# Kernel tuning notes

Hardware: AMD Instinct MI355X
Metric: run time of the kernel (lower is better)

The kernel has to match this reference:

```python
import jax, jax.numpy as jnp
import numpy as np
import math

DIM = 512
HEADS = 8          # dim // num_head_channels = 512 // 64
HEAD_CH = 64
GROUPS = 32        # guided-diffusion normalization() = GroupNorm(32, dim)
EPS = 1e-5
CROSS_DIM = 768


def setup_inputs() -> dict:
    key = jax.random.key(0)
    ks = jax.random.split(key, 8)
    B, C, Hs, Ws, L = 16, DIM, 32, 32, 77
    x = jax.random.normal(ks[0], (B, C, Hs, Ws), dtype=jnp.float32)
    c = jax.random.normal(ks[1], (B, CROSS_DIM, L), dtype=jnp.float32)
    # GroupNorm affine params
    gamma = jnp.ones((C,), jnp.float32)
    beta = jnp.zeros((C,), jnp.float32)
    # 1x1 conv weights stored as [out, in]
    w_qkv = jax.random.normal(ks[2], (3 * C, C), jnp.float32) / math.sqrt(C)
    b_qkv = jnp.zeros((3 * C,), jnp.float32)
    w_c = jax.random.normal(ks[3], (2 * C, CROSS_DIM), jnp.float32) / math.sqrt(CROSS_DIM)
    b_c = jnp.zeros((2 * C,), jnp.float32)
    # NOTE: original proj_out is zero-initialized (zero_module); we use small
    # random weights so the reference exercises non-trivial math end-to-end.
    w_p = jax.random.normal(ks[4], (C, C), jnp.float32) / math.sqrt(C)
    b_p = jnp.zeros((C,), jnp.float32)
    return {"x": x, "c": c, "gamma": gamma, "beta": beta,
            "w_qkv": w_qkv, "b_qkv": b_qkv, "w_c": w_c, "b_c": b_c,
            "w_p": w_p, "b_p": b_p}


def reference(x, c, gamma, beta, w_qkv, b_qkv, w_c, b_c, w_p, b_p):
    B, C, Hs, Ws = x.shape
    T = Hs * Ws
    xf = x.reshape(B, C, T)

    # GroupNorm(32) over (channels_per_group, spatial)
    xg = xf.reshape(B, GROUPS, C // GROUPS, T)
    mean = xg.mean(axis=(2, 3), keepdims=True)
    var = xg.var(axis=(2, 3), keepdims=True)
    xn = ((xg - mean) * jax.lax.rsqrt(var + EPS)).reshape(B, C, T)
    xn = xn * gamma[None, :, None] + beta[None, :, None]

    # qkv 1x1 conv: [B, 3C, T]
    qkv = jnp.einsum('oc,bct->bot', w_qkv, xn) + b_qkv[None, :, None]
    q, k, v = jnp.split(qkv, 3, axis=1)
    q = q.reshape(B, HEADS, HEAD_CH, T)
    k = k.reshape(B, HEADS, HEAD_CH, T)
    v = v.reshape(B, HEADS, HEAD_CH, T)

    # cross-attn cond kv: [B, 2C, L] -> concat on sequence axis
    ckv = jnp.einsum('oc,bcl->bol', w_c, c) + b_c[None, :, None]
    kc, vc = jnp.split(ckv, 2, axis=1)
    L = c.shape[-1]
    k = jnp.concatenate([k, kc.reshape(B, HEADS, HEAD_CH, L)], axis=-1)
    v = jnp.concatenate([v, vc.reshape(B, HEADS, HEAD_CH, L)], axis=-1)

    scale = 1.0 / math.sqrt(HEAD_CH)
    # scores [B, H, T, T+L]; scale applied inside softmax as in FusedSoftmaxMaybeApex
    logits = jnp.einsum('bhct,bhcs->bhts', q, k) * scale
    w = jax.nn.softmax(logits, axis=-1)
    a = jnp.einsum('bhts,bhcs->bhct', w, v).reshape(B, C, T)

    h = jnp.einsum('oc,bct->bot', w_p, a) + b_p[None, :, None]
    return (xf + h).reshape(B, C, Hs, Ws)
```

## Files before the change

kernel.cpp:

```cpp
#include <hip/hip_runtime.h>

#define B_   16
#define C_   512
#define T_   1024
#define H_   8
#define D_   64
#define G_   32
#define L_   77
#define S_   1101
#define SPAD 1152
#define NPAD 51
#define CD_  768
#define BT_  (B_*T_)
#define SROW 72
#define QSC  0.18033688011112042f

typedef __bf16 bf16x8 __attribute__((ext_vector_type(8)));
typedef float  f32x4  __attribute__((ext_vector_type(4)));

static __device__ __forceinline__ unsigned short f2bf(float f) {
    unsigned int u = __float_as_uint(f);
    u = (u + 0x7fffu + ((u >> 16) & 1u)) >> 16;
    return (unsigned short)u;
}

static __device__ __forceinline__ unsigned int pk_bf16(float a, float b) {
    unsigned int d;
    asm("v_cvt_pk_bf16_f32 %0, %1, %2" : "=v"(d) : "v"(a), "v"(b));
    return d;
}

static __device__ __forceinline__ void gload_lds16(const unsigned short* g,
                                                   unsigned short* l) {
    __builtin_amdgcn_global_load_lds(
        (const __attribute__((address_space(1))) unsigned int*)g,
        (__attribute__((address_space(3))) unsigned int*)l, 16, 0, 0);
}

__global__ __launch_bounds__(256) void prep_k(const float* __restrict__ x,
                                              float* __restrict__ stats,
                                              const float* __restrict__ w_qkv,
                                              const float* __restrict__ w_p,
                                              const float* __restrict__ w_c,
                                              const float* __restrict__ cin,
                                              unsigned short* __restrict__ wqkv_pk,
                                              unsigned short* __restrict__ wp_pk,
                                              unsigned short* __restrict__ wc_pk,
                                              unsigned short* __restrict__ cpk) {
    const int tid = threadIdx.x;
    if (blockIdx.x < 512) {
        const int bg = blockIdx.x;
        const float* p = x + (size_t)bg * 16384;
        float s = 0.f, s2 = 0.f;
        for (int i = tid; i < 16384; i += 256) {
            float v = p[i];
            s += v; s2 += v * v;
        }
        __shared__ float rs[256], rs2[256];
        rs[tid] = s; rs2[tid] = s2;
        __syncthreads();
        for (int off = 128; off > 0; off >>= 1) {
            if (tid < off) { rs[tid] += rs[tid + off]; rs2[tid] += rs2[tid + off]; }
            __syncthreads();
        }
        if (tid == 0) {
            float mean = rs[0] * (1.0f / 16384.0f);
            float var  = rs2[0] * (1.0f / 16384.0f) - mean * mean;
            stats[2 * bg]     = mean;
            stats[2 * bg + 1] = rsqrtf(var + 1e-5f);
        }
        return;
    }
    if (blockIdx.x < 1408) {
        const int cid = (blockIdx.x - 512) * 256 + tid;
        const float* src;
        unsigned short* dst;
        if (cid < 98304) {
            const int ml = cid & 127, k8 = (cid >> 7) & 7, kt = (cid >> 10) & 7, mt = cid >> 13;
            src = w_qkv + (size_t)(mt * 128 + ml) * 512 + kt * 64 + k8 * 8;
            dst = wqkv_pk + (size_t)cid * 8;
        } else if (cid < 131072) {
            const int c2 = cid - 98304;
            const int ml = c2 & 127, k8 = (c2 >> 7) & 7, kt = (c2 >> 10) & 7, mt = c2 >> 13;
            src = w_p + (size_t)(mt * 128 + ml) * 512 + kt * 64 + k8 * 8;
            dst = wp_pk + (size_t)c2 * 8;
        } else {
            const int c3 = cid - 131072;
            const int ml = c3 & 127, k8 = (c3 >> 7) & 7;
            const int ktmt = c3 >> 10;
            const int kt = ktmt % 12, mt = ktmt / 12;
            src = w_c + (size_t)(mt * 128 + ml) * 768 + kt * 64 + k8 * 8;
            dst = wc_pk + (size_t)c3 * 8;
        }
        const float4 v0 = *(const float4*)src, v1 = *(const float4*)(src + 4);
        unsigned short tmp[8];
        tmp[0] = f2bf(v0.x); tmp[1] = f2bf(v0.y); tmp[2] = f2bf(v0.z); tmp[3] = f2bf(v0.w);
        tmp[4] = f2bf(v1.x); tmp[5] = f2bf(v1.y); tmp[6] = f2bf(v1.z); tmp[7] = f2bf(v1.w);
        *(uint4*)dst = *(uint4*)tmp;
        return;
    }
    const int idx2 = blockIdx.x - 1408;
    const int kt = idx2 % 12, b = idx2 / 12;
#pragma unroll
    for (int it = 0; it < 4; it++) {
        const int idx = it * 256 + tid;
        const int k8 = idx >> 7, l = idx & 127;
        unsigned short tmp[8];
        const float* src = cin + ((size_t)b * CD_ + kt * 64 + k8 * 8) * L_ + l;
#pragma unroll
        for (int q = 0; q < 8; q++)
            tmp[q] = (l < L_) ? f2bf(src[(size_t)q * L_]) : (unsigned short)0;
        *(uint4*)&cpk[(size_t)b * 98304 + ((size_t)(kt * 8 + k8)) * 1024 + (size_t)l * 8] =
            *(uint4*)tmp;
    }
}

__global__ __launch_bounds__(256) void gn_apply_t(const float* __restrict__ x,
                                                  const float* __restrict__ stats,
                                                  const float* __restrict__ gamma,
                                                  const float* __restrict__ beta,
                                                  unsigned short* __restrict__ xnT) {
    const int t0 = blockIdx.x * 64, kt = blockIdx.y, b = blockIdx.z;
    const int c0 = kt * 64;
    const int tid = threadIdx.x;
    __shared__ float st[64][66];
#pragma unroll
    for (int it = 0; it < 4; it++) {
        const int fid = it * 256 + tid;
        const int ci = fid >> 4, t4 = (fid & 15) * 4;
        const int c = c0 + ci;
        const float4 xv = *(const float4*)&x[((size_t)(b * C_ + c) << 10) + t0 + t4];
        const int bg = b * G_ + (c >> 4);
        const float mean = stats[2 * bg], istd = stats[2 * bg + 1];
        const float gs = gamma[c] * istd, gb = beta[c] - mean * gs;
        st[t4 + 0][ci] = xv.x * gs + gb;
        st[t4 + 1][ci] = xv.y * gs + gb;
        st[t4 + 2][ci] = xv.z * gs + gb;
        st[t4 + 3][ci] = xv.w * gs + gb;
    }
    __syncthreads();
#pragma unroll
    for (int it = 0; it < 2; it++) {
        const int cid = it * 256 + tid;
        const int k8 = cid >> 6, tl = cid & 63;
        const int n = (b << 10) + t0 + tl;
        const int nt = n >> 7, nm = n & 127;
        unsigned short tmp[8];
        const float* src = &st[tl][k8 * 8];
#pragma unroll
        for (int q = 0; q < 8; q++) tmp[q] = f2bf(src[q]);
        *(uint4*)&xnT[(((size_t)nt * 8 + kt) * 8 + k8) * 1024 + (size_t)nm * 8] = *(uint4*)tmp;
    }
}

template<int MODE, int KT>
__global__ __launch_bounds__(256) void mgemm_k(const unsigned short* __restrict__ Apk,
                                               const unsigned short* __restrict__ Bpk,
                                               const float* __restrict__ bias,
                                               const float* __restrict__ resid,
                                               unsigned short* __restrict__ qpk,
                                               unsigned short* __restrict__ kpk,
                                               unsigned short* __restrict__ vpk,
                                               float* __restrict__ outp) {
    __shared__ unsigned short lds[18432];
    const int tid = threadIdx.x, wave = tid >> 6, lane = tid & 63;
    const int quad = lane >> 4, l16 = lane & 15;
    const int nt = blockIdx.x, mt = blockIdx.y;
    const int mw = (wave & 1) * 64, nw = (wave >> 1) * 64;

    f32x4 acc[4][4];
#pragma unroll
    for (int i = 0; i < 4; i++)
#pragma unroll
        for (int j = 0; j < 4; j++) acc[i][j] = (f32x4){0.f, 0.f, 0.f, 0.f};

    const unsigned short* Ab = Apk + (size_t)mt * KT * 8192;
    const unsigned short* Bb = Bpk + ((MODE == 2) ? (size_t)blockIdx.z * KT * 8192 : 0)
                                   + (size_t)nt * KT * 8192;

    for (int kt = 0; kt < KT; kt++) {
        const unsigned short* as = Ab + kt * 8192 + wave * 2048 + lane * 8;
        const unsigned short* bs = Bb + kt * 8192 + wave * 2048 + lane * 8;
        unsigned short* la = lds + wave * 2048;
        unsigned short* lb = lds + 8192 + wave * 2048;
#pragma unroll
        for (int j = 0; j < 4; j++) {
            gload_lds16(as + j * 512, la + j * 512);
            gload_lds16(bs + j * 512, lb + j * 512);
        }
        __syncthreads();
#pragma unroll
        for (int kh = 0; kh < 2; kh++) {
            const int k8 = kh * 4 + quad;
            bf16x8 af[4], bfr[4];
#pragma unroll
            for (int i = 0; i < 4; i++) {
                af[i]  = *(const bf16x8*)&lds[(size_t)(k8 * 128 + mw + i * 16 + l16) * 8];
                bfr[i] = *(const bf16x8*)&lds[8192 + (size_t)(k8 * 128 + nw + i * 16 + l16) * 8];
            }
#pragma unroll
            for (int mi = 0; mi < 4; mi++)
#pragma unroll
                for (int ni = 0; ni < 4; ni++)
                    acc[mi][ni] = __builtin_amdgcn_mfma_f32_16x16x32_bf16(
                        af[mi], bfr[ni], acc[mi][ni], 0, 0, 0);
        }
        __syncthreads();
    }

    const int gm0 = mt * 128 + mw;
    const int gn0 = nt * 128 + nw;

    if (MODE == 1) {
        const int b = gn0 >> 10, t0 = gn0 & 1023;
#pragma unroll
        for (int mi = 0; mi < 4; mi++) {
#pragma unroll
            for (int r = 0; r < 4; r++) {
                const int m = gm0 + mi * 16 + quad * 4 + r;
                const float bv = bias[m];
                const size_t rowb = ((size_t)(b * C_ + m) << 10) + t0;
#pragma unroll
                for (int ni = 0; ni < 4; ni++) {
                    const size_t a = rowb + ni * 16 + l16;
                    outp[a] = acc[mi][ni][r] + bv + resid[a];
                }
            }
        }
        return;
    }

    const int region = gm0 >> 9;
    const int h = (gm0 & 511) >> 6;
    const int b = (MODE == 2) ? blockIdx.z : (gn0 >> 10);
    const int bh = b * 8 + h;
    const bool vregion = (MODE == 0) ? (region == 2) : (region == 1);

    if (!vregion) {
        const float sc = (MODE == 0 && region == 0) ? QSC : 1.0f;
        unsigned short* base;
        int trow0;
        size_t tilestride;
        if (MODE == 0) {
            base = (region == 0) ? qpk + (size_t)bh * 16 * 4096
                                 : kpk + (size_t)bh * 18 * 4096;
            trow0 = gn0 & 1023;
        } else {
            base = kpk + (size_t)(bh * 18 + 16 + (gn0 >> 6)) * 4096;
            trow0 = -1;
        }
        (void)tilestride;
#pragma unroll
        for (int mi = 0; mi < 4; mi++) {
            const int k8 = mi * 2 + (quad >> 1);
            const int sub = (quad & 1) * 4;
#pragma unroll
            for (int ni = 0; ni < 4; ni++) {
                float vv[4];
                bool valid = true;
                if (MODE == 2) valid = (gn0 + ni * 16 + l16) < L_;
#pragma unroll
                for (int r = 0; r < 4; r++)
                    vv[r] = valid ? (acc[mi][ni][r] + bias[gm0 + mi * 16 + quad * 4 + r]) * sc
                                  : 0.f;
                uint2 d;
                d.x = pk_bf16(vv[0], vv[1]);
                d.y = pk_bf16(vv[2], vv[3]);
                unsigned short* dst;
                if (MODE == 0) {
                    const int t = trow0 + ni * 16 + l16;
                    dst = base + (size_t)(t >> 6) * 4096 + ((size_t)k8 * 64 + (t & 63)) * 8 + sub;
                } else {
                    const int row = ni * 16 + l16;
                    dst = base + ((size_t)k8 * 64 + row) * 8 + sub;
                }
                *(uint2*)dst = d;
            }
        }
    } else {
        unsigned short* wlds = lds + wave * 4608;
#pragma unroll
        for (int mi = 0; mi < 4; mi++)
#pragma unroll
            for (int ni = 0; ni < 4; ni++) {
                bool valid = true;
                if (MODE == 2) valid = (gn0 + ni * 16 + l16) < L_;
#pragma unroll
                for (int r = 0; r < 4; r++) {
                    const float v = valid ? acc[mi][ni][r] + bias[gm0 + mi * 16 + quad * 4 + r]
                                          : 0.f;
                    wlds[(mi * 16 + quad * 4 + r) * SROW + ni * 16 + l16] = f2bf(v);
                }
            }
        __syncthreads();
        const int stile = (MODE == 0) ? ((gn0 & 1023) >> 6) : (16 + (gn0 >> 6));
        unsigned short* dst = vpk + (size_t)(bh * 18 + stile) * 4096;
        const int sk8 = lane & 7, cb = lane >> 3;
#pragma unroll
        for (int it = 0; it < 8; it++) {
            const int ch = it * 8 + cb;
            *(uint4*)&dst[((size_t)sk8 * 64 + ch) * 8] =
                *(const uint4*)&wlds[ch * SROW + sk8 * 8];
        }
    }
}

__global__ __launch_bounds__(256, 4) void flash_k(const unsigned short* __restrict__ qpk,
                                                  const unsigned short* __restrict__ kpk,
                                                  const unsigned short* __restrict__ vpk,
                                                  unsigned short* __restrict__ aT) {
    __shared__ __align__(16) unsigned short ks[4096];
    __shared__ __align__(16) unsigned short vs[4096];
    __shared__ __align__(16) unsigned short psA[4 * 32 * SROW];

    const int tid  = threadIdx.x;
    const int wave = tid >> 6, lane = tid & 63;
    const int quad = lane >> 4, l16 = lane & 15;
    const int bh  = blockIdx.x;
    const int b = bh >> 3, h = bh & 7;
    const int qt0 = blockIdx.y * 128;

    const unsigned short* qtb = qpk + ((size_t)bh * 16 + blockIdx.y * 2 + (wave >> 1)) * 4096;
    const int qr0 = (wave & 1) * 32 + l16;
    bf16x8 bq0[2], bq1[2];
#pragma unroll
    for (int s = 0; s < 2; s++) {
        bq0[s] = *(const bf16x8*)&qtb[((size_t)quad * 64 + qr0 + s * 16) * 8];
        bq1[s] = *(const bf16x8*)&qtb[((size_t)(quad + 4) * 64 + qr0 + s * 16) * 8];
    }

    unsigned short* ps = psA + wave * 32 * SROW;

    float rsum[2] = {0.f, 0.f};
    f32x4 o_acc[2][4];
#pragma unroll
    for (int s = 0; s < 2; s++)
#pragma unroll
        for (int nb = 0; nb < 4; nb++) o_acc[s][nb] = (f32x4){0.f, 0.f, 0.f, 0.f};

    for (int stile = 0; stile < 18; stile++) {
        const unsigned short* kt = kpk + ((size_t)bh * 18 + stile) * 4096 + wave * 1024 + lane * 8;
        const unsigned short* vt = vpk + ((size_t)bh * 18 + stile) * 4096 + wave * 1024 + lane * 8;
        unsigned short* lk = ks + wave * 1024;
        unsigned short* lv = vs + wave * 1024;
        gload_lds16(kt, lk);       gload_lds16(kt + 512, lk + 512);
        gload_lds16(vt, lv);       gload_lds16(vt + 512, lv + 512);
        __syncthreads();

        f32x4 sacc[2][4];
#pragma unroll
        for (int sb = 0; sb < 4; sb++) {
            const bf16x8 ak0 = *(const bf16x8*)&ks[((size_t)quad * 64 + sb * 16 + l16) * 8];
            const bf16x8 ak1 = *(const bf16x8*)&ks[((size_t)(quad + 4) * 64 + sb * 16 + l16) * 8];
#pragma unroll
            for (int s = 0; s < 2; s++) {
                f32x4 z = (f32x4){0.f, 0.f, 0.f, 0.f};
                z = __builtin_amdgcn_mfma_f32_16x16x32_bf16(ak0, bq0[s], z, 0, 0, 0);
                z = __builtin_amdgcn_mfma_f32_16x16x32_bf16(ak1, bq1[s], z, 0, 0, 0);
                sacc[s][sb] = z;
            }
        }

#pragma unroll
        for (int s = 0; s < 2; s++) {
#pragma unroll
            for (int sb = 0; sb < 4; sb++) {
                const float e0 = __builtin_exp2f(sacc[s][sb][0]);
                const float e1 = __builtin_exp2f(sacc[s][sb][1]);
                const float e2 = __builtin_exp2f(sacc[s][sb][2]);
                const float e3 = __builtin_exp2f(sacc[s][sb][3]);
                rsum[s] += (e0 + e1) + (e2 + e3);
                uint2 d;
                d.x = pk_bf16(e0, e1);
                d.y = pk_bf16(e2, e3);
                *(uint2*)&ps[(s * 16 + l16) * SROW + sb * 16 + quad * 4] = d;
            }
        }
        asm volatile("s_waitcnt lgkmcnt(0)" ::: "memory");

        bf16x8 ap0[2], ap1[2];
#pragma unroll
        for (int s = 0; s < 2; s++) {
            ap0[s] = *(const bf16x8*)&ps[(s * 16 + l16) * SROW + quad * 8];
            ap1[s] = *(const bf16x8*)&ps[(s * 16 + l16) * SROW + 32 + quad * 8];
        }
#pragma unroll
        for (int nb = 0; nb < 4; nb++) {
            const bf16x8 bv0 = *(const bf16x8*)&vs[((size_t)quad * 64 + nb * 16 + l16) * 8];
            const bf16x8 bv1 = *(const bf16x8*)&vs[((size_t)(quad + 4) * 64 + nb * 16 + l16) * 8];
#pragma unroll
            for (int s = 0; s < 2; s++) {
                o_acc[s][nb] = __builtin_amdgcn_mfma_f32_16x16x32_bf16(ap0[s], bv0, o_acc[s][nb], 0, 0, 0);
                o_acc[s][nb] = __builtin_amdgcn_mfma_f32_16x16x32_bf16(ap1[s], bv1, o_acc[s][nb], 0, 0, 0);
            }
        }
        __syncthreads();
    }

    float linv[2][4];
#pragma unroll
    for (int s = 0; s < 2; s++) {
        float lsum = rsum[s];
        lsum += __shfl_xor(lsum, 16);
        lsum += __shfl_xor(lsum, 32);
#pragma unroll
        for (int r = 0; r < 4; r++) {
            const float lr = __shfl(lsum, quad * 4 + r);
            linv[s][r] = 1.0f / (lr - (float)NPAD);
        }
    }

#pragma unroll
    for (int s = 0; s < 2; s++)
#pragma unroll
        for (int nb = 0; nb < 4; nb++)
#pragma unroll
            for (int r = 0; r < 4; r++)
                ps[(s * 16 + quad * 4 + r) * SROW + nb * 16 + l16] =
                    f2bf(o_acc[s][nb][r] * linv[s][r]);
    asm volatile("s_waitcnt lgkmcnt(0)" ::: "memory");
    const int k8 = lane >> 3;
#pragma unroll
    for (int it = 0; it < 4; it++) {
        const int tl = (lane & 7) + it * 8;
        const int n = (b << 10) + qt0 + wave * 32 + tl;
        const int ntb = n >> 7, nm = n & 127;
        *(uint4*)&aT[(((size_t)ntb * 8 + h) * 8 + k8) * 1024 + (size_t)nm * 8] =
            *(const uint4*)&ps[tl * SROW + k8 * 8];
    }
}

extern "C" void kernel_launch(void* const* d_in, const int* in_sizes, int n_in,
                              void* d_out, int out_size, void* d_ws, size_t ws_size,
                              hipStream_t stream) {
    const float* x     = (const float*)d_in[0];
    const float* cin   = (const float*)d_in[1];
    const float* gamma = (const float*)d_in[2];
    const float* beta  = (const float*)d_in[3];
    const float* w_qkv = (const float*)d_in[4];
    const float* b_qkv = (const float*)d_in[5];
    const float* w_c   = (const float*)d_in[6];
    const float* b_c   = (const float*)d_in[7];
    const float* w_p   = (const float*)d_in[8];
    const float* b_p   = (const float*)d_in[9];
    float* out = (float*)d_out;

    float* ws    = (float*)d_ws;
    float* stats = ws;
    unsigned short* xnT     = (unsigned short*)(ws + 1024);
    unsigned short* wqkv_pk = xnT + 8388608;
    unsigned short* wp_pk   = wqkv_pk + 786432;
    unsigned short* wc_pk   = wp_pk + 262144;
    unsigned short* cpk     = wc_pk + 786432;
    unsigned short* qpk     = cpk + 1572864;
    unsigned short* kpk     = qpk + 8388608;
    unsigned short* vpk     = kpk + 9437184;
    unsigned short* aT      = vpk + 9437184;

    prep_k<<<dim3(1600), 256, 0, stream>>>(x, stats, w_qkv, w_p, w_c, cin,
                                           wqkv_pk, wp_pk, wc_pk, cpk);
    gn_apply_t<<<dim3(16, 8, 16), 256, 0, stream>>>(x, stats, gamma, beta, xnT);
    mgemm_k<0, 8><<<dim3(128, 12), 256, 0, stream>>>(wqkv_pk, xnT, b_qkv, nullptr,
                                                     qpk, kpk, vpk, nullptr);
    mgemm_k<2, 12><<<dim3(1, 8, 16), 256, 0, stream>>>(wc_pk, cpk, b_c, nullptr,
                                                       nullptr, kpk, vpk, nullptr);
    flash_k<<<dim3(128, 8), 256, 0, stream>>>(qpk, kpk, vpk, aT);
    mgemm_k<1, 8><<<dim3(128, 4), 256, 0, stream>>>(wp_pk, aT, b_p, x,
                                                    nullptr, nullptr, nullptr, out);
}
```

Baseline: 268.5 us.

## Double-buffer K/V tiles, enlarge per-wave query tile, swizzle P LDS layout

The flash attention kernel now prefetches the next K/V tile into a second LDS buffer while computing on the current one, removing the load-then-sync stall at the start of each iteration. Each wave now owns 64 query rows instead of 32, which halves the grid and doubles K/V reuse per LDS load. The P/output staging buffer moves from padded rows to an XOR-swizzled 64-wide layout to avoid bank conflicts. This raises register and LDS pressure, so the launch bound drops to 2 blocks per CU, and occupancy falls with fewer blocks overall.

New measurement: 273.7 us. About the same (+1.9%).

```diff
diff --git a/kernel.cpp b/kernel.cpp
--- a/kernel.cpp
+++ b/kernel.cpp
@@ -240,7 +240,6 @@
         const float sc = (MODE == 0 && region == 0) ? QSC : 1.0f;
         unsigned short* base;
         int trow0;
-        size_t tilestride;
         if (MODE == 0) {
             base = (region == 0) ? qpk + (size_t)bh * 16 * 4096
                                  : kpk + (size_t)bh * 18 * 4096;
@@ -249,7 +248,6 @@
             base = kpk + (size_t)(bh * 18 + 16 + (gn0 >> 6)) * 4096;
             trow0 = -1;
         }
-        (void)tilestride;
 #pragma unroll
         for (int mi = 0; mi < 4; mi++) {
             const int k8 = mi * 2 + (quad >> 1);
@@ -305,101 +303,112 @@
     }
 }
 
-__global__ __launch_bounds__(256, 4) void flash_k(const unsigned short* __restrict__ qpk,
+__global__ __launch_bounds__(256, 2) void flash_k(const unsigned short* __restrict__ qpk,
                                                   const unsigned short* __restrict__ kpk,
                                                   const unsigned short* __restrict__ vpk,
                                                   unsigned short* __restrict__ aT) {
-    __shared__ __align__(16) unsigned short ks[4096];
-    __shared__ __align__(16) unsigned short vs[4096];
-    __shared__ __align__(16) unsigned short psA[4 * 32 * SROW];
+    __shared__ __align__(16) unsigned short ks[2][4096];
+    __shared__ __align__(16) unsigned short vs[2][4096];
+    __shared__ __align__(16) unsigned short psA[4 * 64 * 64];
 
     const int tid  = threadIdx.x;
     const int wave = tid >> 6, lane = tid & 63;
     const int quad = lane >> 4, l16 = lane & 15;
     const int bh  = blockIdx.x;
     const int b = bh >> 3, h = bh & 7;
-    const int qt0 = blockIdx.y * 128;
-
-    const unsigned short* qtb = qpk + ((size_t)bh * 16 + blockIdx.y * 2 + (wave >> 1)) * 4096;
-    const int qr0 = (wave & 1) * 32 + l16;
-    bf16x8 bq0[2], bq1[2];
-#pragma unroll
-    for (int s = 0; s < 2; s++) {
-        bq0[s] = *(const bf16x8*)&qtb[((size_t)quad * 64 + qr0 + s * 16) * 8];
-        bq1[s] = *(const bf16x8*)&qtb[((size_t)(quad + 4) * 64 + qr0 + s * 16) * 8];
-    }
-
-    unsigned short* ps = psA + wave * 32 * SROW;
-
-    float rsum[2] = {0.f, 0.f};
-    f32x4 o_acc[2][4];
-#pragma unroll
-    for (int s = 0; s < 2; s++)
+    const int qt = blockIdx.y * 4 + wave;
+
+    const unsigned short* qtb = qpk + ((size_t)bh * 16 + qt) * 4096;
+    bf16x8 bq0[4], bq1[4];
+#pragma unroll
+    for (int s = 0; s < 4; s++) {
+        bq0[s] = *(const bf16x8*)&qtb[((size_t)quad * 64 + s * 16 + l16) * 8];
+        bq1[s] = *(const bf16x8*)&qtb[((size_t)(quad + 4) * 64 + s * 16 + l16) * 8];
+    }
+
+    unsigned short* ps = psA + wave * 4096;
+
+    const unsigned short* kbase = kpk + (size_t)bh * 18 * 4096 + wave * 1024 + lane * 8;
+    const unsigned short* vbase = vpk + (size_t)bh * 18 * 4096 + wave * 1024 + lane * 8;
+
+#define STAGE(p, t) do {                                             \
+        const unsigned short* kg = kbase + (size_t)(t) * 4096;       \
+        const unsigned short* vg = vbase + (size_t)(t) * 4096;       \
+        unsigned short* lkp = &ks[p][wave * 1024];                   \
+        unsigned short* lvp = &vs[p][wave * 1024];                   \
+        gload_lds16(kg, lkp);       gload_lds16(kg + 512, lkp + 512);\
+        gload_lds16(vg, lvp);       gload_lds16(vg + 512, lvp + 512);\
+    } while (0)
+
+    float rsum[4] = {0.f, 0.f, 0.f, 0.f};
+    f32x4 o_acc[4][4];
+#pragma unroll
+    for (int s = 0; s < 4; s++)
 #pragma unroll
         for (int nb = 0; nb < 4; nb++) o_acc[s][nb] = (f32x4){0.f, 0.f, 0.f, 0.f};
 
-    for (int stile = 0; stile < 18; stile++) {
-        const unsigned short* kt = kpk + ((size_t)bh * 18 + stile) * 4096 + wave * 1024 + lane * 8;
-        const unsigned short* vt = vpk + ((size_t)bh * 18 + stile) * 4096 + wave * 1024 + lane * 8;
-        unsigned short* lk = ks + wave * 1024;
-        unsigned short* lv = vs + wave * 1024;
-        gload_lds16(kt, lk);       gload_lds16(kt + 512, lk + 512);
-        gload_lds16(vt, lv);       gload_lds16(vt + 512, lv + 512);
-        __syncthreads();
-
-        f32x4 sacc[2][4];
+    STAGE(0, 0);
+    __syncthreads();
+
+    for (int t = 0; t < 18; t++) {
+        const int p = t & 1;
+        if (t < 17) STAGE(p ^ 1, t + 1);
+        const unsigned short* kb = &ks[p][0];
+        const unsigned short* vb = &vs[p][0];
+
 #pragma unroll
         for (int sb = 0; sb < 4; sb++) {
-            const bf16x8 ak0 = *(const bf16x8*)&ks[((size_t)quad * 64 + sb * 16 + l16) * 8];
-            const bf16x8 ak1 = *(const bf16x8*)&ks[((size_t)(quad + 4) * 64 + sb * 16 + l16) * 8];
-#pragma unroll
-            for (int s = 0; s < 2; s++) {
+            const bf16x8 ak0 = *(const bf16x8*)&kb[((size_t)quad * 64 + sb * 16 + l16) * 8];
+            const bf16x8 ak1 = *(const bf16x8*)&kb[((size_t)(quad + 4) * 64 + sb * 16 + l16) * 8];
+            f32x4 sacc[4];
+#pragma unroll
+            for (int s = 0; s < 4; s++) {
                 f32x4 z = (f32x4){0.f, 0.f, 0.f, 0.f};
                 z = __builtin_amdgcn_mfma_f32_16x16x32_bf16(ak0, bq0[s], z, 0, 0, 0);
                 z = __builtin_amdgcn_mfma_f32_16x16x32_bf16(ak1, bq1[s], z, 0, 0, 0);
-                sacc[s][sb] = z;
-            }
-        }
-
-#pragma unroll
-        for (int s = 0; s < 2; s++) {
-#pragma unroll
-            for (int sb = 0; sb < 4; sb++) {
-                const float e0 = __builtin_exp2f(sacc[s][sb][0]);
-                const float e1 = __builtin_exp2f(sacc[s][sb][1]);
-                const float e2 = __builtin_exp2f(sacc[s][sb][2]);
-                const float e3 = __builtin_exp2f(sacc[s][sb][3]);
+                sacc[s] = z;
+            }
+#pragma unroll
+            for (int s = 0; s < 4; s++) {
+                const float e0 = __builtin_exp2f(sacc[s][0]);
+                const float e1 = __builtin_exp2f(sacc[s][1]);
+                const float e2 = __builtin_exp2f(sacc[s][2]);
+                const float e3 = __builtin_exp2f(sacc[s][3]);
                 rsum[s] += (e0 + e1) + (e2 + e3);
                 uint2 d;
                 d.x = pk_bf16(e0, e1);
                 d.y = pk_bf16(e2, e3);
-                *(uint2*)&ps[(s * 16 + l16) * SROW + sb * 16 + quad * 4] = d;
+                const int row = s * 16 + l16;
+                const int u = 2 * sb + (quad >> 1);
+                *(uint2*)&ps[row * 64 + (((u ^ (row & 7)) << 3) + (quad & 1) * 4)] = d;
             }
         }
         asm volatile("s_waitcnt lgkmcnt(0)" ::: "memory");
 
-        bf16x8 ap0[2], ap1[2];
-#pragma unroll
-        for (int s = 0; s < 2; s++) {
-            ap0[s] = *(const bf16x8*)&ps[(s * 16 + l16) * SROW + quad * 8];
-            ap1[s] = *(const bf16x8*)&ps[(s * 16 + l16) * SROW + 32 + quad * 8];
+        bf16x8 ap0[4], ap1[4];
+#pragma unroll
+        for (int s = 0; s < 4; s++) {
+            const int row = s * 16 + l16;
+            ap0[s] = *(const bf16x8*)&ps[row * 64 + ((quad       ^ (row & 7)) << 3)];
+            ap1[s] = *(const bf16x8*)&ps[row * 64 + (((quad + 4) ^ (row & 7)) << 3)];
         }
 #pragma unroll
         for (int nb = 0; nb < 4; nb++) {
-            const bf16x8 bv0 = *(const bf16x8*)&vs[((size_t)quad * 64 + nb * 16 + l16) * 8];
-            const bf16x8 bv1 = *(const bf16x8*)&vs[((size_t)(quad + 4) * 64 + nb * 16 + l16) * 8];
-#pragma unroll
-            for (int s = 0; s < 2; s++) {
+            const bf16x8 bv0 = *(const bf16x8*)&vb[((size_t)quad * 64 + nb * 16 + l16) * 8];
+            const bf16x8 bv1 = *(const bf16x8*)&vb[((size_t)(quad + 4) * 64 + nb * 16 + l16) * 8];
+#pragma unroll
+            for (int s = 0; s < 4; s++) {
                 o_acc[s][nb] = __builtin_amdgcn_mfma_f32_16x16x32_bf16(ap0[s], bv0, o_acc[s][nb], 0, 0, 0);
                 o_acc[s][nb] = __builtin_amdgcn_mfma_f32_16x16x32_bf16(ap1[s], bv1, o_acc[s][nb], 0, 0, 0);
             }
         }
         __syncthreads();
     }
-
-    float linv[2][4];
-#pragma unroll
-    for (int s = 0; s < 2; s++) {
+#undef STAGE
+
+    float linv[4][4];
+#pragma unroll
+    for (int s = 0; s < 4; s++) {
         float lsum = rsum[s];
         lsum += __shfl_xor(lsum, 16);
         lsum += __shfl_xor(lsum, 32);
@@ -411,22 +420,25 @@
     }
 
 #pragma unroll
-    for (int s = 0; s < 2; s++)
+    for (int s = 0; s < 4; s++)
 #pragma unroll
         for (int nb = 0; nb < 4; nb++)
 #pragma unroll
-            for (int r = 0; r < 4; r++)
-                ps[(s * 16 + quad * 4 + r) * SROW + nb * 16 + l16] =
+            for (int r = 0; r < 4; r++) {
+                const int row = s * 16 + quad * 4 + r;
+                const int col = nb * 16 + l16;
+                ps[row * 64 + ((((col >> 3) ^ (row & 7)) << 3) + (col & 7))] =
                     f2bf(o_acc[s][nb][r] * linv[s][r]);
+            }
     asm volatile("s_waitcnt lgkmcnt(0)" ::: "memory");
     const int k8 = lane >> 3;
 #pragma unroll
-    for (int it = 0; it < 4; it++) {
+    for (int it = 0; it < 8; it++) {
         const int tl = (lane & 7) + it * 8;
-        const int n = (b << 10) + qt0 + wave * 32 + tl;
+        const int n = (b << 10) + qt * 64 + tl;
         const int ntb = n >> 7, nm = n & 127;
         *(uint4*)&aT[(((size_t)ntb * 8 + h) * 8 + k8) * 1024 + (size_t)nm * 8] =
-            *(const uint4*)&ps[tl * SROW + k8 * 8];
+            *(const uint4*)&ps[tl * 64 + ((k8 ^ (tl & 7)) << 3)];
     }
 }
 
@@ -464,7 +476,7 @@
                                                      qpk, kpk, vpk, nullptr);
     mgemm_k<2, 12><<<dim3(1, 8, 16), 256, 0, stream>>>(wc_pk, cpk, b_c, nullptr,
                                                        nullptr, kpk, vpk, nullptr);
-    flash_k<<<dim3(128, 8), 256, 0, stream>>>(qpk, kpk, vpk, aT);
+    flash_k<<<dim3(128, 4), 256, 0, stream>>>(qpk, kpk, vpk, aT);
     mgemm_k<1, 8><<<dim3(128, 4), 256, 0, stream>>>(wp_pk, aT, b_p, x,
                                                     nullptr, nullptr, nullptr, out);
 }
```

## Double-buffer K/V tiles in flash kernel and merge QKV and cond GEMM launches

Applied to the files above, without the earlier changes.

The flash attention loop now prefetches the next K/V tile into a second LDS buffer while computing on the current one. This drops one barrier-wait per tile on global loads. MFMA sections are wrapped in s_setprio raises, and the occupancy hint goes from 4 to 3 blocks to fit the doubled LDS. The QKV GEMM and the cross-condition KV GEMM are fused into a single launch using an extra grid row, which removes one kernel launch and lets the small cond GEMM overlap the large one. The trade-offs are more LDS per block and lower occupancy in the attention kernel.

Measured after the change: 273.1 us. Within noise of the previous version (+1.7%).

```diff
diff --git a/kernel.cpp b/kernel.cpp
--- a/kernel.cpp
+++ b/kernel.cpp
@@ -154,18 +154,18 @@
 }
 
 template<int MODE, int KT>
-__global__ __launch_bounds__(256) void mgemm_k(const unsigned short* __restrict__ Apk,
-                                               const unsigned short* __restrict__ Bpk,
-                                               const float* __restrict__ bias,
-                                               const float* __restrict__ resid,
-                                               unsigned short* __restrict__ qpk,
-                                               unsigned short* __restrict__ kpk,
-                                               unsigned short* __restrict__ vpk,
-                                               float* __restrict__ outp) {
-    __shared__ unsigned short lds[18432];
+static __device__ __forceinline__ void mgemm_body(const unsigned short* __restrict__ Apk,
+                                                  const unsigned short* __restrict__ Bpk,
+                                                  const float* __restrict__ bias,
+                                                  const float* __restrict__ resid,
+                                                  unsigned short* __restrict__ qpk,
+                                                  unsigned short* __restrict__ kpk,
+                                                  unsigned short* __restrict__ vpk,
+                                                  float* __restrict__ outp,
+                                                  unsigned short* lds,
+                                                  const int nt, const int mt, const int zz) {
     const int tid = threadIdx.x, wave = tid >> 6, lane = tid & 63;
     const int quad = lane >> 4, l16 = lane & 15;
-    const int nt = blockIdx.x, mt = blockIdx.y;
     const int mw = (wave & 1) * 64, nw = (wave >> 1) * 64;
 
     f32x4 acc[4][4];
@@ -175,7 +175,7 @@
         for (int j = 0; j < 4; j++) acc[i][j] = (f32x4){0.f, 0.f, 0.f, 0.f};
 
     const unsigned short* Ab = Apk + (size_t)mt * KT * 8192;
-    const unsigned short* Bb = Bpk + ((MODE == 2) ? (size_t)blockIdx.z * KT * 8192 : 0)
+    const unsigned short* Bb = Bpk + ((MODE == 2) ? (size_t)zz * KT * 8192 : 0)
                                    + (size_t)nt * KT * 8192;
 
     for (int kt = 0; kt < KT; kt++) {
@@ -232,7 +232,7 @@
 
     const int region = gm0 >> 9;
     const int h = (gm0 & 511) >> 6;
-    const int b = (MODE == 2) ? blockIdx.z : (gn0 >> 10);
+    const int b = (MODE == 2) ? zz : (gn0 >> 10);
     const int bh = b * 8 + h;
     const bool vregion = (MODE == 0) ? (region == 2) : (region == 1);
 
@@ -240,7 +240,6 @@
         const float sc = (MODE == 0 && region == 0) ? QSC : 1.0f;
         unsigned short* base;
         int trow0;
-        size_t tilestride;
         if (MODE == 0) {
             base = (region == 0) ? qpk + (size_t)bh * 16 * 4096
                                  : kpk + (size_t)bh * 18 * 4096;
@@ -249,7 +248,6 @@
             base = kpk + (size_t)(bh * 18 + 16 + (gn0 >> 6)) * 4096;
             trow0 = -1;
         }
-        (void)tilestride;
 #pragma unroll
         for (int mi = 0; mi < 4; mi++) {
             const int k8 = mi * 2 + (quad >> 1);
@@ -305,12 +303,41 @@
     }
 }
 
-__global__ __launch_bounds__(256, 4) void flash_k(const unsigned short* __restrict__ qpk,
+__global__ __launch_bounds__(256) void mgemm_qkvc_k(const unsigned short* __restrict__ wqkv_pk,
+                                                    const unsigned short* __restrict__ xnT,
+                                                    const float* __restrict__ b_qkv,
+                                                    const unsigned short* __restrict__ wc_pk,
+                                                    const unsigned short* __restrict__ cpk,
+                                                    const float* __restrict__ b_c,
+                                                    unsigned short* __restrict__ qpk,
+                                                    unsigned short* __restrict__ kpk,
+                                                    unsigned short* __restrict__ vpk) {
+    __shared__ unsigned short lds[18432];
+    if (blockIdx.y < 12) {
+        mgemm_body<0, 8>(wqkv_pk, xnT, b_qkv, nullptr, qpk, kpk, vpk, nullptr,
+                         lds, blockIdx.x, blockIdx.y, 0);
+    } else {
+        mgemm_body<2, 12>(wc_pk, cpk, b_c, nullptr, nullptr, kpk, vpk, nullptr,
+                          lds, 0, blockIdx.x & 7, blockIdx.x >> 3);
+    }
+}
+
+__global__ __launch_bounds__(256) void mgemm_proj_k(const unsigned short* __restrict__ Apk,
+                                                    const unsigned short* __restrict__ Bpk,
+                                                    const float* __restrict__ bias,
+                                                    const float* __restrict__ resid,
+                                                    float* __restrict__ outp) {
+    __shared__ unsigned short lds[18432];
+    mgemm_body<1, 8>(Apk, Bpk, bias, resid, nullptr, nullptr, nullptr, outp,
+                     lds, blockIdx.x, blockIdx.y, 0);
+}
+
+__global__ __launch_bounds__(256, 3) void flash_k(const unsigned short* __restrict__ qpk,
                                                   const unsigned short* __restrict__ kpk,
                                                   const unsigned short* __restrict__ vpk,
                                                   unsigned short* __restrict__ aT) {
-    __shared__ __align__(16) unsigned short ks[4096];
-    __shared__ __align__(16) unsigned short vs[4096];
+    __shared__ __align__(16) unsigned short ks[2][4096];
+    __shared__ __align__(16) unsigned short vs[2][4096];
     __shared__ __align__(16) unsigned short psA[4 * 32 * SROW];
 
     const int tid  = threadIdx.x;
@@ -331,6 +358,18 @@
 
     unsigned short* ps = psA + wave * 32 * SROW;
 
+    const unsigned short* kbase = kpk + (size_t)bh * 18 * 4096 + wave * 1024 + lane * 8;
+    const unsigned short* vbase = vpk + (size_t)bh * 18 * 4096 + wave * 1024 + lane * 8;
+
+#define STAGE(p, t) do {                                             \
+        const unsigned short* kg = kbase + (size_t)(t) * 4096;       \
+        const unsigned short* vg = vbase + (size_t)(t) * 4096;       \
+        unsigned short* lkp = &ks[p][wave * 1024];                   \
+        unsigned short* lvp = &vs[p][wave * 1024];                   \
+        gload_lds16(kg, lkp);       gload_lds16(kg + 512, lkp + 512);\
+        gload_lds16(vg, lvp);       gload_lds16(vg + 512, lvp + 512);\
+    } while (0)
+
     float rsum[2] = {0.f, 0.f};
     f32x4 o_acc[2][4];
 #pragma unroll
@@ -338,20 +377,21 @@
 #pragma unroll
         for (int nb = 0; nb < 4; nb++) o_acc[s][nb] = (f32x4){0.f, 0.f, 0.f, 0.f};
 
-    for (int stile = 0; stile < 18; stile++) {
-        const unsigned short* kt = kpk + ((size_t)bh * 18 + stile) * 4096 + wave * 1024 + lane * 8;
-        const unsigned short* vt = vpk + ((size_t)bh * 18 + stile) * 4096 + wave * 1024 + lane * 8;
-        unsigned short* lk = ks + wave * 1024;
-        unsigned short* lv = vs + wave * 1024;
-        gload_lds16(kt, lk);       gload_lds16(kt + 512, lk + 512);
-        gload_lds16(vt, lv);       gload_lds16(vt + 512, lv + 512);
-        __syncthreads();
+    STAGE(0, 0);
+    __syncthreads();
+
+    for (int t = 0; t < 18; t++) {
+        const int p = t & 1;
+        if (t < 17) STAGE(p ^ 1, t + 1);
+        const unsigned short* kb = &ks[p][0];
+        const unsigned short* vb = &vs[p][0];
 
         f32x4 sacc[2][4];
+        __builtin_amdgcn_s_setprio(1);
 #pragma unroll
         for (int sb = 0; sb < 4; sb++) {
-            const bf16x8 ak0 = *(const bf16x8*)&ks[((size_t)quad * 64 + sb * 16 + l16) * 8];
-            const bf16x8 ak1 = *(const bf16x8*)&ks[((size_t)(quad + 4) * 64 + sb * 16 + l16) * 8];
+            const bf16x8 ak0 = *(const bf16x8*)&kb[((size_t)quad * 64 + sb * 16 + l16) * 8];
+            const bf16x8 ak1 = *(const bf16x8*)&kb[((size_t)(quad + 4) * 64 + sb * 16 + l16) * 8];
 #pragma unroll
             for (int s = 0; s < 2; s++) {
                 f32x4 z = (f32x4){0.f, 0.f, 0.f, 0.f};
@@ -360,6 +400,7 @@
                 sacc[s][sb] = z;
             }
         }
+        __builtin_amdgcn_s_setprio(0);
 
 #pragma unroll
         for (int s = 0; s < 2; s++) {
@@ -384,18 +425,21 @@
             ap0[s] = *(const bf16x8*)&ps[(s * 16 + l16) * SROW + quad * 8];
             ap1[s] = *(const bf16x8*)&ps[(s * 16 + l16) * SROW + 32 + quad * 8];
         }
+        __builtin_amdgcn_s_setprio(1);
 #pragma unroll
         for (int nb = 0; nb < 4; nb++) {
-            const bf16x8 bv0 = *(const bf16x8*)&vs[((size_t)quad * 64 + nb * 16 + l16) * 8];
-            const bf16x8 bv1 = *(const bf16x8*)&vs[((size_t)(quad + 4) * 64 + nb * 16 + l16) * 8];
+            const bf16x8 bv0 = *(const bf16x8*)&vb[((size_t)quad * 64 + nb * 16 + l16) * 8];
+            const bf16x8 bv1 = *(const bf16x8*)&vb[((size_t)(quad + 4) * 64 + nb * 16 + l16) * 8];
 #pragma unroll
             for (int s = 0; s < 2; s++) {
                 o_acc[s][nb] = __builtin_amdgcn_mfma_f32_16x16x32_bf16(ap0[s], bv0, o_acc[s][nb], 0, 0, 0);
                 o_acc[s][nb] = __builtin_amdgcn_mfma_f32_16x16x32_bf16(ap1[s], bv1, o_acc[s][nb], 0, 0, 0);
             }
         }
+        __builtin_amdgcn_s_setprio(0);
         __syncthreads();
     }
+#undef STAGE
 
     float linv[2][4];
 #pragma unroll
@@ -460,11 +504,9 @@
     prep_k<<<dim3(1600), 256, 0, stream>>>(x, stats, w_qkv, w_p, w_c, cin,
                                            wqkv_pk, wp_pk, wc_pk, cpk);
     gn_apply_t<<<dim3(16, 8, 16), 256, 0, stream>>>(x, stats, gamma, beta, xnT);
-    mgemm_k<0, 8><<<dim3(128, 12), 256, 0, stream>>>(wqkv_pk, xnT, b_qkv, nullptr,
-                                                     qpk, kpk, vpk, nullptr);
-    mgemm_k<2, 12><<<dim3(1, 8, 16), 256, 0, stream>>>(wc_pk, cpk, b_c, nullptr,
-                                                       nullptr, kpk, vpk, nullptr);
+    mgemm_qkvc_k<<<dim3(128, 13), 256, 0, stream>>>(wqkv_pk, xnT, b_qkv,
+                                                    wc_pk, cpk, b_c,
+                                                    qpk, kpk, vpk);
     flash_k<<<dim3(128, 8), 256, 0, stream>>>(qpk, kpk, vpk, aT);
-    mgemm_k<1, 8><<<dim3(128, 4), 256, 0, stream>>>(wp_pk, aT, b_p, x,
-                                                    nullptr, nullptr, nullptr, out);
-}
+    mgemm_proj_k<<<dim3(128, 4), 256, 0, stream>>>(wp_pk, aT, b_p, x, out);
+}
```
